# Kernel tuning notes

Hardware: AMD Instinct MI355X
Metric: run time of the kernel (lower is better)

Reference implementation:

```python
import jax, jax.numpy as jnp
import numpy as np

B, T, D, H = 1, 2049, 1024, 16
HD = D // H                      # head_dim = 64
MAX_SEQ = 1025
L = 2 * MAX_SEQ - 1              # = T (required by the module's relative shift)

def setup_inputs() -> dict:
    key = jax.random.key(0)
    ks = jax.random.split(key, 12)
    s = 0.02
    return {
        'q': jax.random.normal(ks[0], (B, T, D), dtype=jnp.float32),
        'k': jax.random.normal(ks[1], (B, T, D), dtype=jnp.float32),
        'v': jax.random.normal(ks[2], (B, T, D), dtype=jnp.float32),
        'mask': jnp.tril(jnp.ones((1, 1, T, T), dtype=jnp.int32)),  # causal
        'Wq_w': jax.random.normal(ks[3], (D, D), dtype=jnp.float32) * s,
        'Wq_b': jnp.zeros((D,), dtype=jnp.float32),
        'Wk_w': jax.random.normal(ks[4], (D, D), dtype=jnp.float32) * s,
        'Wk_b': jnp.zeros((D,), dtype=jnp.float32),
        'Wv_w': jax.random.normal(ks[5], (D, D), dtype=jnp.float32) * s,
        'Wv_b': jnp.zeros((D,), dtype=jnp.float32),
        'Er': jax.random.normal(ks[6], (L, HD), dtype=jnp.float32),
        'Wo_w': jax.random.normal(ks[7], (D, D), dtype=jnp.float32) * s,
        'Wo_b': jnp.zeros((D,), dtype=jnp.float32),
    }

def reference(q, k, v, mask, Wq_w, Wq_b, Wk_w, Wk_b, Wv_w, Wv_b, Er, Wo_w, Wo_b):
    b, t, d = q.shape
    def proj(x, w, bias):
        # nn.Linear: x @ W^T + b ; then (B,T,H,HD) -> (B,H,T,HD)
        return (x @ w.T + bias).reshape(b, t, H, HD).transpose(0, 2, 1, 3)
    qh = proj(q, Wq_w, Wq_b)
    kh = proj(k, Wk_w, Wk_b)
    vh = proj(v, Wv_w, Wv_b)
    scores = jnp.einsum('bhtd,bhsd->bhts', qh, kh)          # (B,H,T,T)
    QEr = jnp.einsum('bhtd,ld->bhtl', qh, Er)               # (B,H,T,L) with L == T
    # _relative_shift: pad a zero row on seq dim then drop first row ->
    # row i becomes QEr row i+1, last row zeros (faithful to torch code)
    rel = jnp.concatenate([QEr[:, :, 1:, :], jnp.zeros_like(QEr[:, :, :1, :])], axis=2)
    scores = scores + rel
    scores = jnp.where(mask[:, :, :t, :t] == 0, -jnp.inf, scores)
    attn = jax.nn.softmax(scores / (HD ** 0.5), axis=-1)
    ctx = jnp.einsum('bhts,bhsd->bthd', attn, vh).reshape(b, t, d)
    return ctx @ Wo_w.T + Wo_b
```

## Files before the change

kernel.cpp:

```cpp
#include <hip/hip_runtime.h>
#include <hip/hip_bf16.h>
#include <math.h>

constexpr int T_SEQ = 2049;
constexpr int D_MODEL = 1024;
constexpr int N_HEAD = 16;
constexpr int HEAD_DIM = 64;
constexpr int VT_STRIDE = 2112;
constexpr int T1_ROWS = 1152;

typedef __attribute__((ext_vector_type(8))) short short8;
typedef __attribute__((ext_vector_type(4))) short short4v;
typedef __attribute__((ext_vector_type(4))) float floatx4;

__device__ inline void load_lds16(const void* g, void* l) {
  __builtin_amdgcn_global_load_lds(
      (const __attribute__((address_space(1))) unsigned int*)g,
      (__attribute__((address_space(3))) unsigned int*)l, 16, 0, 0);
}

__device__ inline short8 cvt8_bf16(const float* p) {
  float4 a = *(const float4*)p, b = *(const float4*)(p + 4);
  __hip_bfloat16 t[8] = {__float2bfloat16(a.x), __float2bfloat16(a.y),
                         __float2bfloat16(a.z), __float2bfloat16(a.w),
                         __float2bfloat16(b.x), __float2bfloat16(b.y),
                         __float2bfloat16(b.z), __float2bfloat16(b.w)};
  return *(const short8*)t;
}

__device__ inline float bf2f(__hip_bfloat16 x) { return __bfloat162float(x); }

__global__ __launch_bounds__(256) void cast_bf16x(
    const float* __restrict__ i0, const float* __restrict__ i1,
    const float* __restrict__ i2, const float* __restrict__ i3,
    __hip_bfloat16* __restrict__ o0, __hip_bfloat16* __restrict__ o1,
    __hip_bfloat16* __restrict__ o2, __hip_bfloat16* __restrict__ o3, int n) {
  const int z = blockIdx.y;
  const float* in = z == 0 ? i0 : z == 1 ? i1 : z == 2 ? i2 : i3;
  __hip_bfloat16* out = z == 0 ? o0 : z == 1 ? o1 : z == 2 ? o2 : o3;
  const int i = (blockIdx.x * 256 + threadIdx.x) * 8;
  if (i + 8 > n) return;
  *(short8*)(out + i) = cvt8_bf16(in + i);
}

__global__ __launch_bounds__(256) void cast_bf16_one(const float* __restrict__ in,
                                                     __hip_bfloat16* __restrict__ out,
                                                     int n) {
  const int i = (blockIdx.x * 256 + threadIdx.x) * 8;
  if (i + 8 > n) return;
  *(short8*)(out + i) = cvt8_bf16(in + i);
}

template <int BN, int OUTK>
__global__ __launch_bounds__(256) void mfma_gemm(
    const __hip_bfloat16* __restrict__ A0, const __hip_bfloat16* __restrict__ A1,
    const __hip_bfloat16* __restrict__ A2, const __hip_bfloat16* __restrict__ W0,
    const __hip_bfloat16* __restrict__ W1, const __hip_bfloat16* __restrict__ W2,
    const float* __restrict__ bias0, const float* __restrict__ bias1,
    const float* __restrict__ bias2, void* C0, void* C1, void* C2, int M) {
  constexpr int K = D_MODEL;
  constexpr int NT = BN / 32;
  __shared__ __align__(16) __hip_bfloat16 As[128 * 32];
  __shared__ __align__(16) __hip_bfloat16 Bs[BN * 32];

  const int z = blockIdx.z;
  const short* A = (const short*)(z == 0 ? A0 : z == 1 ? A1 : A2);
  const short* W = (const short*)(z == 0 ? W0 : z == 1 ? W1 : W2);
  const float* bias = z == 0 ? bias0 : z == 1 ? bias1 : bias2;
  void* C = z == 0 ? C0 : z == 1 ? C1 : C2;

  const int tid = threadIdx.x;
  const int wave = tid >> 6, lane = tid & 63;
  const int col = lane & 15, quad = lane >> 4;
  const int wm = wave >> 1, wn = wave & 1;
  const int m0 = blockIdx.y * 128, n0 = blockIdx.x * BN;

  const int sr = lane >> 2;
  const int ss = lane & 3;
  const int sch = ss ^ ((sr >> 1) & 3);

  floatx4 acc[4][NT];
#pragma unroll
  for (int i = 0; i < 4; i++)
#pragma unroll
    for (int j = 0; j < NT; j++) acc[i][j] = (floatx4){0.f, 0.f, 0.f, 0.f};

  for (int k0 = 0; k0 < K; k0 += 32) {
    if (k0) __syncthreads();
#pragma unroll
    for (int i = 0; i < 2; i++) {
      const int rb = wave * 32 + i * 16;
      const int am = min(m0 + rb + sr, M - 1);
      load_lds16(A + (size_t)am * K + k0 + sch * 8, (char*)As + rb * 64);
    }
#pragma unroll
    for (int i = 0; i < BN / 64; i++) {
      const int rb = (wave * (BN / 64) + i) * 16;
      const int bn = n0 + rb + sr;
      load_lds16(W + (size_t)bn * K + k0 + sch * 8, (char*)Bs + rb * 64);
    }
    __syncthreads();

    short8 af[4], bf[NT];
#pragma unroll
    for (int t = 0; t < 4; t++) {
      const int ra = wm * 64 + t * 16 + col;
      af[t] = *(const short8*)(As + ra * 32 + (quad ^ ((ra >> 1) & 3)) * 8);
    }
#pragma unroll
    for (int t = 0; t < NT; t++) {
      const int rb = wn * (BN / 2) + t * 16 + col;
      bf[t] = *(const short8*)(Bs + rb * 32 + (quad ^ ((rb >> 1) & 3)) * 8);
    }
#pragma unroll
    for (int mt = 0; mt < 4; mt++)
#pragma unroll
      for (int nt = 0; nt < NT; nt++)
        acc[mt][nt] =
            __builtin_amdgcn_mfma_f32_16x16x32_bf16(af[mt], bf[nt], acc[mt][nt], 0, 0, 0);
  }

#pragma unroll
  for (int mt = 0; mt < 4; mt++) {
#pragma unroll
    for (int r = 0; r < 4; r++) {
      const int m = m0 + wm * 64 + mt * 16 + quad * 4 + r;
      if (m >= M) continue;
#pragma unroll
      for (int nt = 0; nt < NT; nt++) {
        const int n = n0 + wn * (BN / 2) + nt * 16 + col;
        const float val = acc[mt][nt][r] + bias[n];
        if (OUTK == 0) {
          ((float*)C)[(size_t)m * D_MODEL + n] = val;
        } else {
          if (z < 2) {
            const int h = n >> 6, hd = n & 63;
            ((__hip_bfloat16*)C)[((size_t)h * T_SEQ + m) * HEAD_DIM + hd] =
                __float2bfloat16(val);
          } else {
            ((__hip_bfloat16*)C)[(size_t)m * D_MODEL + n] = __float2bfloat16(val);
          }
        }
      }
    }
  }
}

__global__ __launch_bounds__(256) void transpose_v(const __hip_bfloat16* __restrict__ vpr,
                                                   __hip_bfloat16* __restrict__ vt) {
  __shared__ __align__(16) __hip_bfloat16 tile[64][72];
  const int t0 = blockIdx.x * 64;
  const int h = blockIdx.y;
  const int tid = threadIdx.x;
  const short* plane = (const short*)vpr;
  short* oplane = (short*)(vt + (size_t)h * HEAD_DIM * VT_STRIDE);

  for (int idx = tid; idx < 64 * 8; idx += 256) {
    const int row = idx >> 3, ch = idx & 7;
    const int t = t0 + row;
    short8 v = {0, 0, 0, 0, 0, 0, 0, 0};
    if (t < T_SEQ) v = *(const short8*)(plane + (size_t)t * D_MODEL + h * 64 + ch * 8);
    *(short8*)&tile[row][ch * 8] = v;
  }
  __syncthreads();
  for (int idx = tid; idx < 64 * 8; idx += 256) {
    const int d = idx >> 3, ch = idx & 7;
    short8 v;
#pragma unroll
    for (int i = 0; i < 8; i++) v[i] = *(const short*)&tile[ch * 8 + i][d];
    *(short8*)(oplane + (size_t)d * VT_STRIDE + t0 + ch * 8) = v;
  }
}

__global__ __launch_bounds__(512, 4) void flash_attn(
    const __hip_bfloat16* __restrict__ qh, const __hip_bfloat16* __restrict__ kh,
    const __hip_bfloat16* __restrict__ er, const __hip_bfloat16* __restrict__ vt,
    __hip_bfloat16* __restrict__ O0, __hip_bfloat16* __restrict__ O1,
    float* __restrict__ l0g, float* __restrict__ l1g) {
  __shared__ __align__(16) __hip_bfloat16 Ks[2][64 * 128];
  __shared__ __align__(16) __hip_bfloat16 Vs[2][64 * 64];
  __shared__ __align__(16) __hip_bfloat16 Ps[8][1024];

  const int tid = threadIdx.x;
  const int h = blockIdx.y;
  const int b = blockIdx.x;

  const int qt = (b < 8) ? b : 8 + ((b - 8) >> 1);
  const int tq0 = qt * 128;
  const int jmax = min(tq0 + 127, T_SEQ - 1) >> 6;
  int j0, j1;
  bool alt;
  if (b < 8) {
    j0 = 0; j1 = jmax; alt = false;
  } else {
    const int mid = (jmax + 1) >> 1;
    alt = (b - 8) & 1;
    j0 = alt ? mid : 0;
    j1 = alt ? jmax : mid - 1;
  }

  const int wave = tid >> 6;
  const int lane = tid & 63;
  const int col = lane & 15;
  const int quad = lane >> 4;

  const short* qplane = (const short*)(qh + (size_t)h * T_SEQ * HEAD_DIM);
  const short* kplane = (const short*)(kh + (size_t)h * T_SEQ * HEAD_DIM);
  const short* eplane = (const short*)er;
  const short* vplane = (const short*)(vt + (size_t)h * HEAD_DIM * VT_STRIDE);

  const int t_abs = tq0 + wave * 16 + col;
  const int tload = min(t_abs, T_SEQ - 1);
  const bool hiz = (t_abs >= T_SEQ - 1);
  short8 aq[4];
#pragma unroll
  for (int kc = 0; kc < 4; kc++) {
    short8 v = *(const short8*)(qplane + (size_t)tload * 64 + kc * 32 + quad * 8);
    if (kc >= 2 && hiz) v = (short8){0, 0, 0, 0, 0, 0, 0, 0};
    aq[kc] = v;
  }

  floatx4 o[4];
  float l_lane = 0.f;
#pragma unroll
  for (int i = 0; i < 4; i++) o[i] = (floatx4){0.f, 0.f, 0.f, 0.f};

  const int tstrip = tq0 + wave * 16;
  __hip_bfloat16* psw = &Ps[wave][0];

#define STAGE_TILE(JJ, BUF)                                                        \
  {                                                                                \
    const int s0_ = (JJ) * 64;                                                     \
    _Pragma("unroll") for (int ii = 0; ii < 2; ii++) {                             \
      const int i_ = wave * 2 + ii;                                                \
      const int r_ = i_ * 4 + (lane >> 4);                                         \
      const int sl_ = lane & 15;                                                   \
      const int g_ = (sl_ & 8) | ((sl_ ^ (r_ & 7)) & 7);                           \
      const int s_ = min(s0_ + r_, T_SEQ - 1);                                     \
      const short* src_ = (g_ < 8) ? (kplane + (size_t)s_ * 64 + g_ * 8)           \
                                   : (eplane + (size_t)s_ * 64 + (g_ - 8) * 8);    \
      load_lds16(src_, (char*)&Ks[BUF][0] + i_ * 1024);                            \
    }                                                                              \
    {                                                                              \
      const int d_ = wave * 8 + (lane >> 3);                                       \
      const int sl_ = lane & 7;                                                    \
      const int g_ = sl_ ^ (d_ & 7);                                               \
      load_lds16(vplane + (size_t)d_ * VT_STRIDE + s0_ + g_ * 8,                   \
                 (char*)&Vs[BUF][0] + wave * 1024);                                \
    }                                                                              \
  }

  STAGE_TILE(j0, 0)
  int buf = 0;

  for (int j = j0; j <= j1; ++j, buf ^= 1) {
    __syncthreads();
    if (j < j1) STAGE_TILE(j + 1, buf ^ 1)

    const int s0 = j * 64;
    if (s0 > tstrip + 15) continue;

    const __hip_bfloat16* ks = &Ks[buf][0];
    const __hip_bfloat16* vs = &Vs[buf][0];

    floatx4 sacc[4];
#pragma unroll
    for (int st = 0; st < 4; st++) {
      floatx4 c = {0.f, 0.f, 0.f, 0.f};
      const int row = st * 16 + col;
#pragma unroll
      for (int kc = 0; kc < 4; kc++) {
        const int ch = kc * 4 + quad;
        const int slot = (ch & 8) | ((ch ^ (row & 7)) & 7);
        short8 ka = *(const short8*)(ks + row * 128 + slot * 8);
        c = __builtin_amdgcn_mfma_f32_16x16x32_bf16(ka, aq[kc], c, 0, 0, 0);
      }
      sacc[st] = c;
    }

    if (s0 + 63 > tstrip) {
#pragma unroll
      for (int st = 0; st < 4; st++) {
        const int sbase = s0 + st * 16 + quad * 4;
#pragma unroll
        for (int r = 0; r < 4; r++)
          if (sbase + r > t_abs) sacc[st][r] = -INFINITY;
      }
    }

    float rs = 0.f;
#pragma unroll
    for (int st = 0; st < 4; st++)
#pragma unroll
      for (int r = 0; r < 4; r++) {
        const float p = __expf(sacc[st][r] * 0.125f);
        sacc[st][r] = p;
        rs += p;
      }
    l_lane += rs;

#pragma unroll
    for (int st = 0; st < 4; st++) {
      __hip_bfloat16 pb[4];
#pragma unroll
      for (int r = 0; r < 4; r++) pb[r] = __float2bfloat16(sacc[st][r]);
      const int kcA = st >> 1;
      const int quadA = (st & 1) * 2 + (quad >> 1);
      const int off = ((kcA * 4 + quadA) * 16 + col) * 8 + (quad & 1) * 4;
      *(short4v*)(psw + off) = *(const short4v*)pb;
    }
    short8 pa[2];
#pragma unroll
    for (int kc = 0; kc < 2; kc++)
      pa[kc] = *(const short8*)(psw + ((kc * 4 + quad) * 16 + col) * 8);

#pragma unroll
    for (int nt = 0; nt < 4; nt++) {
      const int row = nt * 16 + col;
#pragma unroll
      for (int kc = 0; kc < 2; kc++) {
        const int slot = (kc * 4 + quad) ^ (row & 7);
        short8 vb = *(const short8*)(vs + row * 64 + slot * 8);
        o[nt] = __builtin_amdgcn_mfma_f32_16x16x32_bf16(pa[kc], vb, o[nt], 0, 0, 0);
      }
    }
  }

  l_lane += __shfl_xor(l_lane, 16, 64);
  l_lane += __shfl_xor(l_lane, 32, 64);
  if (lane < 16) {
    const int t = tstrip + lane;
    if (t < T_SEQ) {
      if (!alt)
        l0g[h * T_SEQ + t] = l_lane;
      else
        l1g[h * T1_ROWS + (t - 1024)] = l_lane;
    }
  }
#pragma unroll
  for (int r = 0; r < 4; r++) {
    const int t = tstrip + quad * 4 + r;
    if (t < T_SEQ) {
      if (!alt) {
#pragma unroll
        for (int nt = 0; nt < 4; nt++)
          O0[(size_t)t * D_MODEL + h * 64 + nt * 16 + col] = __float2bfloat16(o[nt][r]);
      } else {
#pragma unroll
        for (int nt = 0; nt < 4; nt++)
          O1[(size_t)(t - 1024) * D_MODEL + h * 64 + nt * 16 + col] =
              __float2bfloat16(o[nt][r]);
      }
    }
  }
}

__global__ __launch_bounds__(256) void finalize(
    const __hip_bfloat16* __restrict__ O0, const __hip_bfloat16* __restrict__ O1,
    const float* __restrict__ l0g, const float* __restrict__ l1g,
    __hip_bfloat16* __restrict__ ctx) {
  const int idx = blockIdx.x * 256 + threadIdx.x;
  if (idx >= T_SEQ * 128) return;
  const int t = idx >> 7;
  const int ch = idx & 127;
  const int h = ch >> 3;

  float l = l0g[h * T_SEQ + t];
  const __hip_bfloat16* a = O0 + (size_t)t * D_MODEL + ch * 8;
  float acc[8];
#pragma unroll
  for (int i = 0; i < 8; i++) acc[i] = bf2f(a[i]);
  if (t >= 1024) {
    l += l1g[h * T1_ROWS + (t - 1024)];
    const __hip_bfloat16* bsrc = O1 + (size_t)(t - 1024) * D_MODEL + ch * 8;
#pragma unroll
    for (int i = 0; i < 8; i++) acc[i] += bf2f(bsrc[i]);
  }
  const float inv = 1.0f / l;
  __hip_bfloat16 outv[8];
#pragma unroll
  for (int i = 0; i < 8; i++) outv[i] = __float2bfloat16(acc[i] * inv);
  *(short8*)(ctx + (size_t)t * D_MODEL + ch * 8) = *(const short8*)outv;
}

extern "C" void kernel_launch(void* const* d_in, const int* in_sizes, int n_in,
                              void* d_out, int out_size, void* d_ws, size_t ws_size,
                              hipStream_t stream) {
  const float* q = (const float*)d_in[0];
  const float* k = (const float*)d_in[1];
  const float* v = (const float*)d_in[2];
  const float* Wq_w = (const float*)d_in[4];
  const float* Wq_b = (const float*)d_in[5];
  const float* Wk_w = (const float*)d_in[6];
  const float* Wk_b = (const float*)d_in[7];
  const float* Wv_w = (const float*)d_in[8];
  const float* Wv_b = (const float*)d_in[9];
  const float* Er = (const float*)d_in[10];
  const float* Wo_w = (const float*)d_in[11];
  const float* Wo_b = (const float*)d_in[12];
  float* out = (float*)d_out;

  char* ws = (char*)d_ws;
  const size_t sz_plane = (size_t)T_SEQ * D_MODEL * 2;
  const size_t sz_w = (size_t)D_MODEL * D_MODEL * 2;
  __hip_bfloat16* qbf = (__hip_bfloat16*)ws;
  __hip_bfloat16* kbf = (__hip_bfloat16*)(ws + sz_plane);
  __hip_bfloat16* vbf = (__hip_bfloat16*)(ws + 2 * sz_plane);
  char* wbase = ws + 3 * sz_plane;
  __hip_bfloat16* wob = (__hip_bfloat16*)(wbase);
  __hip_bfloat16* wqb = (__hip_bfloat16*)(wbase + sz_w);
  __hip_bfloat16* wkb = (__hip_bfloat16*)(wbase + 2 * sz_w);
  __hip_bfloat16* wvb = (__hip_bfloat16*)(wbase + 3 * sz_w);
  char* pbase = wbase + 4 * sz_w;
  __hip_bfloat16* qpr = (__hip_bfloat16*)(pbase);
  __hip_bfloat16* kpr = (__hip_bfloat16*)(pbase + sz_plane);
  __hip_bfloat16* vpr = (__hip_bfloat16*)(pbase + 2 * sz_plane);

  const size_t sz_vt = (size_t)N_HEAD * HEAD_DIM * VT_STRIDE * 2;
  const size_t sz_er = (size_t)T_SEQ * HEAD_DIM * 2;
  const size_t sz_O0 = (size_t)T_SEQ * D_MODEL * 2;
  const size_t sz_O1 = (size_t)T1_ROWS * D_MODEL * 2;
  const size_t sz_l0 = (size_t)N_HEAD * T_SEQ * 4;
  __hip_bfloat16* vt = (__hip_bfloat16*)ws;
  __hip_bfloat16* er_bf = (__hip_bfloat16*)(ws + sz_vt);
  __hip_bfloat16* O0 = (__hip_bfloat16*)(ws + sz_vt + sz_er);
  __hip_bfloat16* O1 = (__hip_bfloat16*)(ws + sz_vt + sz_er + sz_O0);
  float* l0g = (float*)(ws + sz_vt + sz_er + sz_O0 + sz_O1);
  float* l1g = (float*)(ws + sz_vt + sz_er + sz_O0 + sz_O1 + sz_l0);
  __hip_bfloat16* ctxb = (__hip_bfloat16*)(wbase + sz_w);

  const dim3 blk(256);
  const int n_in_elems = T_SEQ * D_MODEL;
  const int n_w_elems = D_MODEL * D_MODEL;
  const int n_er = T_SEQ * HEAD_DIM;

  cast_bf16x<<<dim3((n_in_elems + 2047) / 2048, 3), blk, 0, stream>>>(
      q, k, v, q, qbf, kbf, vbf, qbf, n_in_elems);
  cast_bf16x<<<dim3(n_w_elems / 2048, 4), blk, 0, stream>>>(
      Wq_w, Wk_w, Wv_w, Wo_w, wqb, wkb, wvb, wob, n_w_elems);

  mfma_gemm<128, 2><<<dim3(8, 17, 3), blk, 0, stream>>>(
      qbf, kbf, vbf, wqb, wkb, wvb, Wq_b, Wk_b, Wv_b, qpr, kpr, vpr, T_SEQ);

  cast_bf16_one<<<dim3((n_er + 2047) / 2048), blk, 0, stream>>>(Er, er_bf, n_er);
  transpose_v<<<dim3(33, N_HEAD), blk, 0, stream>>>(vpr, vt);

  flash_attn<<<dim3(26, N_HEAD), dim3(512), 0, stream>>>(qpr, kpr, er_bf, vt, O0, O1,
                                                         l0g, l1g);

  finalize<<<dim3((T_SEQ * 128 + 255) / 256), blk, 0, stream>>>(O0, O1, l0g, l1g, ctxb);

  mfma_gemm<64, 0><<<dim3(16, 17, 1), blk, 0, stream>>>(
      ctxb, ctxb, ctxb, wob, wob, wob, Wo_b, Wo_b, Wo_b, out, out, out, T_SEQ);
}
```

Baseline: 215.3 us.

## Merge cast launches, deepen GEMM K-tile, and normalize unsplit attention rows in-kernel

Folds all input and weight fp32-to-bf16 casts into one launch, and folds the Er cast into the V transpose kernel, to cut launch count. Doubles the GEMM K step to 64 with a new XOR swizzle so there are half as many barriers per K loop. Query tiles that are not split across two blocks now normalize and write the context directly, so the finalize pass only touches the split rows above 1024. The partial-output buffers shrink to match. Larger LDS tiles may lower GEMM occupancy.

```diff
diff --git a/kernel.cpp b/kernel.cpp
--- a/kernel.cpp
+++ b/kernel.cpp
@@ -30,22 +30,27 @@
 
 __device__ inline float bf2f(__hip_bfloat16 x) { return __bfloat162float(x); }
 
-__global__ __launch_bounds__(256) void cast_bf16x(
-    const float* __restrict__ i0, const float* __restrict__ i1,
-    const float* __restrict__ i2, const float* __restrict__ i3,
-    __hip_bfloat16* __restrict__ o0, __hip_bfloat16* __restrict__ o1,
-    __hip_bfloat16* __restrict__ o2, __hip_bfloat16* __restrict__ o3, int n) {
+__global__ __launch_bounds__(256) void cast_all(
+    const float* __restrict__ q, const float* __restrict__ k,
+    const float* __restrict__ v, const float* __restrict__ wq,
+    const float* __restrict__ wk, const float* __restrict__ wv,
+    const float* __restrict__ wo, __hip_bfloat16* __restrict__ qo,
+    __hip_bfloat16* __restrict__ ko, __hip_bfloat16* __restrict__ vo,
+    __hip_bfloat16* __restrict__ wqo, __hip_bfloat16* __restrict__ wko,
+    __hip_bfloat16* __restrict__ wvo, __hip_bfloat16* __restrict__ woo) {
   const int z = blockIdx.y;
-  const float* in = z == 0 ? i0 : z == 1 ? i1 : z == 2 ? i2 : i3;
-  __hip_bfloat16* out = z == 0 ? o0 : z == 1 ? o1 : z == 2 ? o2 : o3;
-  const int i = (blockIdx.x * 256 + threadIdx.x) * 8;
-  if (i + 8 > n) return;
-  *(short8*)(out + i) = cvt8_bf16(in + i);
-}
-
-__global__ __launch_bounds__(256) void cast_bf16_one(const float* __restrict__ in,
-                                                     __hip_bfloat16* __restrict__ out,
-                                                     int n) {
+  const float* in;
+  __hip_bfloat16* out;
+  int n;
+  switch (z) {
+    case 0: in = q; out = qo; n = T_SEQ * D_MODEL; break;
+    case 1: in = k; out = ko; n = T_SEQ * D_MODEL; break;
+    case 2: in = v; out = vo; n = T_SEQ * D_MODEL; break;
+    case 3: in = wq; out = wqo; n = D_MODEL * D_MODEL; break;
+    case 4: in = wk; out = wko; n = D_MODEL * D_MODEL; break;
+    case 5: in = wv; out = wvo; n = D_MODEL * D_MODEL; break;
+    default: in = wo; out = woo; n = D_MODEL * D_MODEL; break;
+  }
   const int i = (blockIdx.x * 256 + threadIdx.x) * 8;
   if (i + 8 > n) return;
   *(short8*)(out + i) = cvt8_bf16(in + i);
@@ -60,8 +65,8 @@
     const float* __restrict__ bias2, void* C0, void* C1, void* C2, int M) {
   constexpr int K = D_MODEL;
   constexpr int NT = BN / 32;
-  __shared__ __align__(16) __hip_bfloat16 As[128 * 32];
-  __shared__ __align__(16) __hip_bfloat16 Bs[BN * 32];
+  __shared__ __align__(16) __hip_bfloat16 As[128 * 64];
+  __shared__ __align__(16) __hip_bfloat16 Bs[BN * 64];
 
   const int z = blockIdx.z;
   const short* A = (const short*)(z == 0 ? A0 : z == 1 ? A1 : A2);
@@ -75,9 +80,9 @@
   const int wm = wave >> 1, wn = wave & 1;
   const int m0 = blockIdx.y * 128, n0 = blockIdx.x * BN;
 
-  const int sr = lane >> 2;
-  const int ss = lane & 3;
-  const int sch = ss ^ ((sr >> 1) & 3);
+  const int srow = lane >> 3;
+  const int sslot = lane & 7;
+  const int sch = sslot ^ srow;
 
   floatx4 acc[4][NT];
 #pragma unroll
@@ -85,39 +90,42 @@
 #pragma unroll
     for (int j = 0; j < NT; j++) acc[i][j] = (floatx4){0.f, 0.f, 0.f, 0.f};
 
-  for (int k0 = 0; k0 < K; k0 += 32) {
+  for (int k0 = 0; k0 < K; k0 += 64) {
     if (k0) __syncthreads();
 #pragma unroll
-    for (int i = 0; i < 2; i++) {
-      const int rb = wave * 32 + i * 16;
-      const int am = min(m0 + rb + sr, M - 1);
-      load_lds16(A + (size_t)am * K + k0 + sch * 8, (char*)As + rb * 64);
-    }
-#pragma unroll
-    for (int i = 0; i < BN / 64; i++) {
-      const int rb = (wave * (BN / 64) + i) * 16;
-      const int bn = n0 + rb + sr;
-      load_lds16(W + (size_t)bn * K + k0 + sch * 8, (char*)Bs + rb * 64);
+    for (int i = 0; i < 4; i++) {
+      const int rb = (wave * 4 + i) * 8;
+      const int am = min(m0 + rb + srow, M - 1);
+      load_lds16(A + (size_t)am * K + k0 + sch * 8, (char*)As + rb * 128);
+    }
+#pragma unroll
+    for (int i = 0; i < BN / 32; i++) {
+      const int rb = (wave * (BN / 32) + i) * 8;
+      const int bn = n0 + rb + srow;
+      load_lds16(W + (size_t)bn * K + k0 + sch * 8, (char*)Bs + rb * 128);
     }
     __syncthreads();
 
-    short8 af[4], bf[NT];
-#pragma unroll
-    for (int t = 0; t < 4; t++) {
-      const int ra = wm * 64 + t * 16 + col;
-      af[t] = *(const short8*)(As + ra * 32 + (quad ^ ((ra >> 1) & 3)) * 8);
-    }
-#pragma unroll
-    for (int t = 0; t < NT; t++) {
-      const int rb = wn * (BN / 2) + t * 16 + col;
-      bf[t] = *(const short8*)(Bs + rb * 32 + (quad ^ ((rb >> 1) & 3)) * 8);
-    }
-#pragma unroll
-    for (int mt = 0; mt < 4; mt++)
-#pragma unroll
-      for (int nt = 0; nt < NT; nt++)
-        acc[mt][nt] =
-            __builtin_amdgcn_mfma_f32_16x16x32_bf16(af[mt], bf[nt], acc[mt][nt], 0, 0, 0);
+#pragma unroll
+    for (int kk = 0; kk < 2; kk++) {
+      short8 af[4], bf[NT];
+#pragma unroll
+      for (int t = 0; t < 4; t++) {
+        const int ra = wm * 64 + t * 16 + col;
+        af[t] = *(const short8*)(As + ra * 64 + ((kk * 4 + quad) ^ (ra & 7)) * 8);
+      }
+#pragma unroll
+      for (int t = 0; t < NT; t++) {
+        const int rb = wn * (BN / 2) + t * 16 + col;
+        bf[t] = *(const short8*)(Bs + rb * 64 + ((kk * 4 + quad) ^ (rb & 7)) * 8);
+      }
+#pragma unroll
+      for (int mt = 0; mt < 4; mt++)
+#pragma unroll
+        for (int nt = 0; nt < NT; nt++)
+          acc[mt][nt] = __builtin_amdgcn_mfma_f32_16x16x32_bf16(af[mt], bf[nt],
+                                                                acc[mt][nt], 0, 0, 0);
+    }
   }
 
 #pragma unroll
@@ -146,12 +154,20 @@
   }
 }
 
-__global__ __launch_bounds__(256) void transpose_v(const __hip_bfloat16* __restrict__ vpr,
-                                                   __hip_bfloat16* __restrict__ vt) {
+__global__ __launch_bounds__(256) void transpose_v_er(
+    const __hip_bfloat16* __restrict__ vpr, __hip_bfloat16* __restrict__ vt,
+    const float* __restrict__ Er, __hip_bfloat16* __restrict__ er_bf) {
+  const int tid = threadIdx.x;
+  if (blockIdx.y == 16) {
+    const int i = (blockIdx.x * 256 + tid) * 8;
+    if (i + 8 <= T_SEQ * HEAD_DIM) *(short8*)(er_bf + i) = cvt8_bf16(Er + i);
+    return;
+  }
+  if (blockIdx.x >= 33) return;
+
   __shared__ __align__(16) __hip_bfloat16 tile[64][72];
   const int t0 = blockIdx.x * 64;
   const int h = blockIdx.y;
-  const int tid = threadIdx.x;
   const short* plane = (const short*)vpr;
   short* oplane = (short*)(vt + (size_t)h * HEAD_DIM * VT_STRIDE);
 
@@ -175,8 +191,9 @@
 __global__ __launch_bounds__(512, 4) void flash_attn(
     const __hip_bfloat16* __restrict__ qh, const __hip_bfloat16* __restrict__ kh,
     const __hip_bfloat16* __restrict__ er, const __hip_bfloat16* __restrict__ vt,
-    __hip_bfloat16* __restrict__ O0, __hip_bfloat16* __restrict__ O1,
-    float* __restrict__ l0g, float* __restrict__ l1g) {
+    __hip_bfloat16* __restrict__ ctx, __hip_bfloat16* __restrict__ O0,
+    __hip_bfloat16* __restrict__ O1, float* __restrict__ l0g,
+    float* __restrict__ l1g) {
   __shared__ __align__(16) __hip_bfloat16 Ks[2][64 * 128];
   __shared__ __align__(16) __hip_bfloat16 Vs[2][64 * 64];
   __shared__ __align__(16) __hip_bfloat16 Ps[8][1024];
@@ -328,28 +345,38 @@
 
   l_lane += __shfl_xor(l_lane, 16, 64);
   l_lane += __shfl_xor(l_lane, 32, 64);
-  if (lane < 16) {
-    const int t = tstrip + lane;
-    if (t < T_SEQ) {
-      if (!alt)
-        l0g[h * T_SEQ + t] = l_lane;
-      else
-        l1g[h * T1_ROWS + (t - 1024)] = l_lane;
-    }
-  }
-#pragma unroll
-  for (int r = 0; r < 4; r++) {
-    const int t = tstrip + quad * 4 + r;
-    if (t < T_SEQ) {
-      if (!alt) {
+
+  if (b < 8) {
+    const float linv = 1.0f / l_lane;
+    float linv_r[4];
+#pragma unroll
+    for (int r = 0; r < 4; r++) linv_r[r] = __shfl(linv, quad * 4 + r, 64);
+#pragma unroll
+    for (int r = 0; r < 4; r++) {
+      const int t = tstrip + quad * 4 + r;
+#pragma unroll
+      for (int nt = 0; nt < 4; nt++)
+        ctx[(size_t)t * D_MODEL + h * 64 + nt * 16 + col] =
+            __float2bfloat16(o[nt][r] * linv_r[r]);
+    }
+  } else {
+    if (lane < 16) {
+      const int t = tstrip + lane;
+      if (t < T_SEQ) {
+        if (!alt)
+          l0g[h * T1_ROWS + (t - 1024)] = l_lane;
+        else
+          l1g[h * T1_ROWS + (t - 1024)] = l_lane;
+      }
+    }
+#pragma unroll
+    for (int r = 0; r < 4; r++) {
+      const int t = tstrip + quad * 4 + r;
+      if (t < T_SEQ) {
+        __hip_bfloat16* dst = (!alt ? O0 : O1) + (size_t)(t - 1024) * D_MODEL;
 #pragma unroll
         for (int nt = 0; nt < 4; nt++)
-          O0[(size_t)t * D_MODEL + h * 64 + nt * 16 + col] = __float2bfloat16(o[nt][r]);
-      } else {
-#pragma unroll
-        for (int nt = 0; nt < 4; nt++)
-          O1[(size_t)(t - 1024) * D_MODEL + h * 64 + nt * 16 + col] =
-              __float2bfloat16(o[nt][r]);
+          dst[h * 64 + nt * 16 + col] = __float2bfloat16(o[nt][r]);
       }
     }
   }
@@ -360,26 +387,20 @@
     const float* __restrict__ l0g, const float* __restrict__ l1g,
     __hip_bfloat16* __restrict__ ctx) {
   const int idx = blockIdx.x * 256 + threadIdx.x;
-  if (idx >= T_SEQ * 128) return;
-  const int t = idx >> 7;
+  const int tr = idx >> 7;
+  const int t = 1024 + tr;
+  if (t >= T_SEQ) return;
   const int ch = idx & 127;
   const int h = ch >> 3;
 
-  float l = l0g[h * T_SEQ + t];
-  const __hip_bfloat16* a = O0 + (size_t)t * D_MODEL + ch * 8;
-  float acc[8];
-#pragma unroll
-  for (int i = 0; i < 8; i++) acc[i] = bf2f(a[i]);
-  if (t >= 1024) {
-    l += l1g[h * T1_ROWS + (t - 1024)];
-    const __hip_bfloat16* bsrc = O1 + (size_t)(t - 1024) * D_MODEL + ch * 8;
-#pragma unroll
-    for (int i = 0; i < 8; i++) acc[i] += bf2f(bsrc[i]);
-  }
+  const float l = l0g[h * T1_ROWS + tr] + l1g[h * T1_ROWS + tr];
+  const __hip_bfloat16* a = O0 + (size_t)tr * D_MODEL + ch * 8;
+  const __hip_bfloat16* bsrc = O1 + (size_t)tr * D_MODEL + ch * 8;
   const float inv = 1.0f / l;
   __hip_bfloat16 outv[8];
 #pragma unroll
-  for (int i = 0; i < 8; i++) outv[i] = __float2bfloat16(acc[i] * inv);
+  for (int i = 0; i < 8; i++)
+    outv[i] = __float2bfloat16((bf2f(a[i]) + bf2f(bsrc[i])) * inv);
   *(short8*)(ctx + (size_t)t * D_MODEL + ch * 8) = *(const short8*)outv;
 }
 
@@ -418,37 +439,30 @@
 
   const size_t sz_vt = (size_t)N_HEAD * HEAD_DIM * VT_STRIDE * 2;
   const size_t sz_er = (size_t)T_SEQ * HEAD_DIM * 2;
-  const size_t sz_O0 = (size_t)T_SEQ * D_MODEL * 2;
-  const size_t sz_O1 = (size_t)T1_ROWS * D_MODEL * 2;
-  const size_t sz_l0 = (size_t)N_HEAD * T_SEQ * 4;
+  const size_t sz_Op = (size_t)T1_ROWS * D_MODEL * 2;
+  const size_t sz_l = (size_t)N_HEAD * T1_ROWS * 4;
   __hip_bfloat16* vt = (__hip_bfloat16*)ws;
   __hip_bfloat16* er_bf = (__hip_bfloat16*)(ws + sz_vt);
   __hip_bfloat16* O0 = (__hip_bfloat16*)(ws + sz_vt + sz_er);
-  __hip_bfloat16* O1 = (__hip_bfloat16*)(ws + sz_vt + sz_er + sz_O0);
-  float* l0g = (float*)(ws + sz_vt + sz_er + sz_O0 + sz_O1);
-  float* l1g = (float*)(ws + sz_vt + sz_er + sz_O0 + sz_O1 + sz_l0);
+  __hip_bfloat16* O1 = (__hip_bfloat16*)(ws + sz_vt + sz_er + sz_Op);
+  float* l0g = (float*)(ws + sz_vt + sz_er + 2 * sz_Op);
+  float* l1g = (float*)(ws + sz_vt + sz_er + 2 * sz_Op + sz_l);
   __hip_bfloat16* ctxb = (__hip_bfloat16*)(wbase + sz_w);
 
   const dim3 blk(256);
-  const int n_in_elems = T_SEQ * D_MODEL;
-  const int n_w_elems = D_MODEL * D_MODEL;
-  const int n_er = T_SEQ * HEAD_DIM;
-
-  cast_bf16x<<<dim3((n_in_elems + 2047) / 2048, 3), blk, 0, stream>>>(
-      q, k, v, q, qbf, kbf, vbf, qbf, n_in_elems);
-  cast_bf16x<<<dim3(n_w_elems / 2048, 4), blk, 0, stream>>>(
-      Wq_w, Wk_w, Wv_w, Wo_w, wqb, wkb, wvb, wob, n_w_elems);
+
+  cast_all<<<dim3(1025, 7), blk, 0, stream>>>(q, k, v, Wq_w, Wk_w, Wv_w, Wo_w, qbf,
+                                              kbf, vbf, wqb, wkb, wvb, wob);
 
   mfma_gemm<128, 2><<<dim3(8, 17, 3), blk, 0, stream>>>(
       qbf, kbf, vbf, wqb, wkb, wvb, Wq_b, Wk_b, Wv_b, qpr, kpr, vpr, T_SEQ);
 
-  cast_bf16_one<<<dim3((n_er + 2047) / 2048), blk, 0, stream>>>(Er, er_bf, n_er);
-  transpose_v<<<dim3(33, N_HEAD), blk, 0, stream>>>(vpr, vt);
-
-  flash_attn<<<dim3(26, N_HEAD), dim3(512), 0, stream>>>(qpr, kpr, er_bf, vt, O0, O1,
-                                                         l0g, l1g);
-
-  finalize<<<dim3((T_SEQ * 128 + 255) / 256), blk, 0, stream>>>(O0, O1, l0g, l1g, ctxb);
+  transpose_v_er<<<dim3(65, 17), blk, 0, stream>>>(vpr, vt, Er, er_bf);
+
+  flash_attn<<<dim3(26, N_HEAD), dim3(512), 0, stream>>>(qpr, kpr, er_bf, vt, ctxb,
+                                                         O0, O1, l0g, l1g);
+
+  finalize<<<dim3((1025 * 128 + 255) / 256), blk, 0, stream>>>(O0, O1, l0g, l1g, ctxb);
 
   mfma_gemm<64, 0><<<dim3(16, 17, 1), blk, 0, stream>>>(
       ctxb, ctxb, ctxb, wob, wob, wob, Wo_b, Wo_b, Wo_b, out, out, out, T_SEQ);
```

After: 204.2 us. -5.2%, faster.
